# Optimization experiments

Hardware: AMD Instinct MI355X
Metric: run time of the kernel (lower is better)

Reference implementation:

```python
import jax, jax.numpy as jnp
import numpy as np

B, C, HW, SCALE = 8, 512, 64, 8
M = C // SCALE  # Q/K channel dim
EPS = 1e-6


def setup_inputs() -> dict:
    key = jax.random.key(0)
    ks = jax.random.split(key, 8)
    s = 0.02
    return {
        "x": jax.random.normal(ks[0], (B, C, HW, HW), dtype=jnp.float32),
        "wq": jax.random.normal(ks[1], (M, C), dtype=jnp.float32) * s,
        "bq": jax.random.normal(ks[2], (M,), dtype=jnp.float32) * s,
        "wk": jax.random.normal(ks[3], (M, C), dtype=jnp.float32) * s,
        "bk": jax.random.normal(ks[4], (M,), dtype=jnp.float32) * s,
        "wv": jax.random.normal(ks[5], (C, C), dtype=jnp.float32) * s,
        "bv": jax.random.normal(ks[6], (C,), dtype=jnp.float32) * s,
        "gamma": jax.random.normal(ks[7], (1,), dtype=jnp.float32),
    }


def reference(x, wq, bq, wk, bk, wv, bv, gamma):
    b, c, w, h = x.shape
    n = w * h
    xf = x.reshape(b, c, n)  # [B,C,N]
    # 1x1 convs == channel GEMMs
    Q = jnp.einsum('bcn,mc->bmn', xf, wq) + bq[None, :, None]  # [B,M,N]
    K = jnp.einsum('bcn,mc->bmn', xf, wk) + bk[None, :, None]  # [B,M,N]
    V = jnp.einsum('bcn,oc->bon', xf, wv) + bv[None, :, None]  # [B,C,N]
    # pooling gate: global max + global avg over spatial dims -> [B,C,1]
    gate = (jnp.max(xf, axis=-1) + jnp.mean(xf, axis=-1))[:, :, None]
    V = gate * V
    Qf = jax.nn.softplus(Q).transpose(0, 2, 1)  # [B,N,M]
    Kf = jax.nn.softplus(K)                      # [B,M,N]
    KV = jnp.einsum('bmn,bcn->bmc', Kf, V)       # [B,M,C]
    norm = 1.0 / jnp.einsum('bnm,bm->bn', Qf, jnp.sum(Kf, axis=-1) + EPS)  # [B,N]
    wval = jnp.einsum('bnm,bmc,bn->bcn', Qf, KV, norm)  # [B,C,N]
    wval = wval.reshape(b, c, h, w)
    return x + gamma * wval
```

## Files before the change

kernel.cpp:

```cpp
#include <hip/hip_runtime.h>
#include <math.h>

#define Bb 8
#define Cc 512
#define Nn 4096
#define Mm 64
#define OC 640
#define EPSf 1e-6f

typedef unsigned short ushort_t;
typedef unsigned int uint_t;
typedef __attribute__((ext_vector_type(8))) short short8;
typedef __attribute__((ext_vector_type(4))) float f32x4;

constexpr size_t OFF_GATE = 0;
constexpr size_t OFF_BCAT = OFF_GATE + (size_t)Bb * Cc;
constexpr size_t OFF_GPM  = OFF_BCAT + (size_t)OC;
constexpr size_t OFF_GPS  = OFF_GPM + (size_t)64 * Bb * Cc;
constexpr size_t OFF_WBF  = OFF_GPS + (size_t)64 * Bb * Cc;
constexpr size_t OFF_XT   = OFF_WBF + (size_t)OC * Cc / 2;
constexpr size_t OFF_QT   = OFF_XT + (size_t)Bb * Nn * Cc / 2;
constexpr size_t OFF_KBF  = OFF_QT + (size_t)Bb * Mm * Nn / 2;
constexpr size_t OFF_VBF  = OFF_KBF + (size_t)Bb * Mm * Nn / 2;
constexpr size_t OFF_KVBF = OFF_VBF + (size_t)Bb * Cc * Nn / 2;
constexpr size_t OFF_KSUM = OFF_KVBF + (size_t)Bb * Cc * Mm / 2;

__device__ __forceinline__ float softplus_f(float v) {
    return fmaxf(v, 0.f) + __logf(1.f + __expf(-fabsf(v)));
}
__device__ __forceinline__ ushort_t f2bf(float f) {
    uint_t u = __float_as_uint(f);
    uint_t r = (u + 0x7fffu + ((u >> 16) & 1u)) >> 16;
    return (ushort_t)r;
}
__device__ __forceinline__ float bf2f(ushort_t h) {
    return __uint_as_float(((uint_t)h) << 16);
}
__device__ __forceinline__ void gload_lds16(const void* g, void* l) {
    __builtin_amdgcn_global_load_lds(
        (const __attribute__((address_space(1))) unsigned int*)g,
        (__attribute__((address_space(3))) unsigned int*)l, 16, 0, 0);
}
#define BARRIER()   asm volatile("s_barrier" ::: "memory")
#define WAIT_VM(N)  asm volatile("s_waitcnt vmcnt(" #N ")" ::: "memory")

__global__ void wconv_k(const float* __restrict__ wq, const float* __restrict__ bq,
                        const float* __restrict__ wk, const float* __restrict__ bk,
                        const float* __restrict__ wv, const float* __restrict__ bv,
                        ushort_t* __restrict__ wbf, float* __restrict__ bcat) {
    int i = blockIdx.x * 256 + threadIdx.x;
    if (i < OC * Cc) {
        int o = i / Cc, c = i % Cc;
        float v;
        if (o < Mm)            v = wq[o * Cc + c];
        else if (o < 2 * Mm)   v = wk[(o - Mm) * Cc + c];
        else                   v = wv[(o - 2 * Mm) * Cc + c];
        wbf[i] = f2bf(v);
    }
    if (i < OC) {
        float v;
        if (i < Mm)            v = bq[i];
        else if (i < 2 * Mm)   v = bk[i - Mm];
        else                   v = bv[i - 2 * Mm];
        bcat[i] = v;
    }
}

__global__ __launch_bounds__(256) void xtrans_k(const float* __restrict__ x, ushort_t* __restrict__ xT,
                                                float* __restrict__ gpm, float* __restrict__ gps) {
    const int nb = blockIdx.x * 64;
    const int cb = blockIdx.y * 64;
    const int b  = blockIdx.z;
    __shared__ float Xt[64][65];
    __shared__ float pmx[4][64], psm[4][64];
    const int t = threadIdx.x;
    #pragma unroll
    for (int it = 0; it < 4; it++) {
        int cl = it * 16 + (t >> 4);
        int n0 = (t & 15) * 4;
        float4 v = *(const float4*)(x + ((size_t)b * Cc + cb + cl) * Nn + nb + n0);
        Xt[cl][n0 + 0] = v.x;
        Xt[cl][n0 + 1] = v.y;
        Xt[cl][n0 + 2] = v.z;
        Xt[cl][n0 + 3] = v.w;
    }
    __syncthreads();
    #pragma unroll
    for (int r = 0; r < 8; r++) {
        int nl = (t >> 5) + r * 8;
        int c0 = (t & 31) * 2;
        uint_t pk = (uint_t)f2bf(Xt[c0][nl]) | ((uint_t)f2bf(Xt[c0 + 1][nl]) << 16);
        *(uint_t*)(xT + ((size_t)b * Nn + nb + nl) * Cc + cb + c0) = pk;
    }
    {
        int cl = t & 63, q = t >> 6;
        float mx = -3.4e38f, sm = 0.f;
        #pragma unroll
        for (int j = 0; j < 16; j++) {
            float v = Xt[cl][q * 16 + j];
            mx = fmaxf(mx, v); sm += v;
        }
        pmx[q][cl] = mx; psm[q][cl] = sm;
    }
    __syncthreads();
    if (t < 64) {
        float mx = fmaxf(fmaxf(pmx[0][t], pmx[1][t]), fmaxf(pmx[2][t], pmx[3][t]));
        float sm = psm[0][t] + psm[1][t] + psm[2][t] + psm[3][t];
        size_t idx = (size_t)blockIdx.x * (Bb * Cc) + (size_t)b * Cc + cb + t;
        gpm[idx] = mx;
        gps[idx] = sm;
    }
}

__global__ void gatered_k(const float* __restrict__ gpm, const float* __restrict__ gps,
                          float* __restrict__ gate) {
    int bc = blockIdx.x;
    int l = threadIdx.x;
    float mx = gpm[(size_t)l * (Bb * Cc) + bc];
    float sm = gps[(size_t)l * (Bb * Cc) + bc];
    #pragma unroll
    for (int off = 32; off; off >>= 1) {
        mx = fmaxf(mx, __shfl_xor(mx, off));
        sm += __shfl_xor(sm, off);
    }
    if (l == 0) gate[bc] = mx + sm * (1.f / Nn);
}

__global__ __launch_bounds__(256, 4) void qkv_mfma_k(const ushort_t* __restrict__ wbf,
                                                     const ushort_t* __restrict__ xT,
                                                     const float* __restrict__ bcat,
                                                     ushort_t* __restrict__ QT,
                                                     ushort_t* __restrict__ Kbf,
                                                     ushort_t* __restrict__ Vbf) {
    const int nb  = blockIdx.x * 128;
    const int oty = blockIdx.y;
    const int b   = blockIdx.z;
    __shared__ ushort_t At[3][2048];
    __shared__ ushort_t Bt[3][4096];
    const int tid  = threadIdx.x;
    const int w    = tid >> 6;
    const int lane = tid & 63;
    const int wr   = w >> 1, wc = w & 1;
    const int hi   = lane >> 4, lo = lane & 15;
    const int rA   = tid >> 2;
    const int kc   = (((tid & 3) ^ ((tid >> 3) & 3)) * 8);
    const int sx   = (hi ^ ((lo >> 1) & 3)) * 8;
    const ushort_t* xb = xT + ((size_t)b * Nn + nb) * Cc;
    const ushort_t* wb = wbf + (size_t)oty * 64 * Cc;

    f32x4 acc[2][4] = {};

    auto stage = [&](int buf, int kb) {
        gload_lds16(wb + (size_t)rA * Cc + kb + kc,        &At[buf][w * 512]);
        gload_lds16(xb + (size_t)rA * Cc + kb + kc,        &Bt[buf][w * 512]);
        gload_lds16(xb + (size_t)(64 + rA) * Cc + kb + kc, &Bt[buf][2048 + w * 512]);
    };
    auto compute = [&](int buf) {
        short8 a[2], bfr[4];
        #pragma unroll
        for (int mi = 0; mi < 2; mi++)
            a[mi] = *(const short8*)(&At[buf][(wr * 32 + mi * 16 + lo) * 32 + sx]);
        #pragma unroll
        for (int ni = 0; ni < 4; ni++)
            bfr[ni] = *(const short8*)(&Bt[buf][(wc * 64 + ni * 16 + lo) * 32 + sx]);
        #pragma unroll
        for (int mi = 0; mi < 2; mi++)
            #pragma unroll
            for (int ni = 0; ni < 4; ni++)
                acc[mi][ni] = __builtin_amdgcn_mfma_f32_16x16x32_bf16(a[mi], bfr[ni], acc[mi][ni], 0, 0, 0);
    };

    stage(0, 0);
    stage(1, 32);
    #pragma unroll
    for (int t = 0; t < 16; ++t) {
        if (t < 15) { WAIT_VM(3); } else { WAIT_VM(0); }
        BARRIER();
        if (t + 2 < 16) stage((t + 2) % 3, (t + 2) * 32);
        compute(t % 3);
    }

    if (oty == 0) {
        ushort_t* qt = QT + ((size_t)b * Nn + nb + wc * 64) * Mm + wr * 32 + hi * 4;
        #pragma unroll
        for (int mi = 0; mi < 2; mi++) {
            const int mb = wr * 32 + mi * 16 + hi * 4;
            #pragma unroll
            for (int ni = 0; ni < 4; ni++) {
                const int n = ni * 16 + lo;
                float s0 = softplus_f(acc[mi][ni][0] + bcat[mb + 0]);
                float s1 = softplus_f(acc[mi][ni][1] + bcat[mb + 1]);
                float s2 = softplus_f(acc[mi][ni][2] + bcat[mb + 2]);
                float s3 = softplus_f(acc[mi][ni][3] + bcat[mb + 3]);
                uint2 pk;
                pk.x = (uint_t)f2bf(s0) | ((uint_t)f2bf(s1) << 16);
                pk.y = (uint_t)f2bf(s2) | ((uint_t)f2bf(s3) << 16);
                *(uint2*)(qt + (size_t)n * Mm + mi * 16) = pk;
            }
        }
    } else if (oty == 1) {
        #pragma unroll
        for (int mi = 0; mi < 2; mi++)
            #pragma unroll
            for (int r = 0; r < 4; r++) {
                const int ol = wr * 32 + mi * 16 + hi * 4 + r;
                const float bias = bcat[Mm + ol];
                ushort_t* dst = Kbf + ((size_t)b * Mm + ol) * Nn + nb + wc * 64;
                #pragma unroll
                for (int ni = 0; ni < 4; ni++)
                    dst[ni * 16 + lo] = f2bf(softplus_f(acc[mi][ni][r] + bias));
            }
    } else {
        const int cbase = (oty - 2) * 64;
        #pragma unroll
        for (int mi = 0; mi < 2; mi++)
            #pragma unroll
            for (int r = 0; r < 4; r++) {
                const int ol = wr * 32 + mi * 16 + hi * 4 + r;
                const float bias = bcat[oty * 64 + ol];
                ushort_t* dst = Vbf + ((size_t)b * Cc + cbase + ol) * Nn + nb + wc * 64;
                #pragma unroll
                for (int ni = 0; ni < 4; ni++)
                    dst[ni * 16 + lo] = f2bf(acc[mi][ni][r] + bias);
            }
    }
}

__global__ __launch_bounds__(256) void ksum_k(const ushort_t* __restrict__ Kbf, float* __restrict__ Ksum) {
    int bm = blockIdx.x;
    const ushort_t* row = Kbf + (size_t)bm * Nn;
    int t = threadIdx.x;
    float sm = 0.f;
    for (int i = t * 8; i < Nn; i += 2048) {
        short8 v = *(const short8*)(row + i);
        #pragma unroll
        for (int j = 0; j < 8; j++) sm += bf2f((ushort_t)v[j]);
    }
    #pragma unroll
    for (int off = 32; off; off >>= 1) sm += __shfl_xor(sm, off);
    __shared__ float ssm[4];
    if ((t & 63) == 0) ssm[t >> 6] = sm;
    __syncthreads();
    if (t == 0) Ksum[bm] = ssm[0] + ssm[1] + ssm[2] + ssm[3];
}

__global__ __launch_bounds__(256, 4) void kv_mfma_k(const ushort_t* __restrict__ Kbf,
                                                    const ushort_t* __restrict__ Vbf,
                                                    float* __restrict__ KVpart) {
    const int cb = blockIdx.x * 128;
    const int split = blockIdx.y;
    const int b = blockIdx.z;
    __shared__ ushort_t Vt[3][4096];
    __shared__ ushort_t Kt[3][2048];
    const int tid = threadIdx.x;
    const int w = tid >> 6, lane = tid & 63;
    const int hi = lane >> 4, lo = lane & 15;
    const int rwl = lane >> 2;
    const int kc  = (((lane & 3) ^ ((lane >> 3) & 3)) * 8);
    const int sx  = (hi ^ ((lo >> 1) & 3)) * 8;
    const ushort_t* Vb = Vbf + (size_t)b * Cc * Nn;
    const ushort_t* Kb = Kbf + (size_t)b * Mm * Nn;
    const int nbase = split * 512;

    f32x4 acc[2][4] = {};

    auto stage = [&](int buf, int n0) {
        #pragma unroll
        for (int li = 0; li < 2; li++) {
            const int rw = (w * 2 + li) * 16 + rwl;
            gload_lds16(Vb + (size_t)(cb + rw) * Nn + n0 + kc, &Vt[buf][(w * 2 + li) * 512]);
        }
        gload_lds16(Kb + (size_t)(w * 16 + rwl) * Nn + n0 + kc, &Kt[buf][w * 512]);
    };
    auto compute = [&](int buf) {
        short8 a[2], bv[4];
        #pragma unroll
        for (int mi = 0; mi < 2; mi++)
            a[mi] = *(const short8*)(&Vt[buf][(w * 32 + mi * 16 + lo) * 32 + sx]);
        #pragma unroll
        for (int ni = 0; ni < 4; ni++)
            bv[ni] = *(const short8*)(&Kt[buf][(ni * 16 + lo) * 32 + sx]);
        #pragma unroll
        for (int mi = 0; mi < 2; mi++)
            #pragma unroll
            for (int ni = 0; ni < 4; ni++)
                acc[mi][ni] = __builtin_amdgcn_mfma_f32_16x16x32_bf16(a[mi], bv[ni], acc[mi][ni], 0, 0, 0);
    };

    stage(0, nbase);
    stage(1, nbase + 32);
    #pragma unroll
    for (int t = 0; t < 16; ++t) {
        if (t < 15) { WAIT_VM(3); } else { WAIT_VM(0); }
        BARRIER();
        if (t + 2 < 16) stage((t + 2) % 3, nbase + (t + 2) * 32);
        compute(t % 3);
    }

    float* dst = KVpart + (size_t)(split * Bb + b) * Cc * Mm;
    #pragma unroll
    for (int mi = 0; mi < 2; mi++)
        #pragma unroll
        for (int r = 0; r < 4; r++) {
            const int c = cb + w * 32 + mi * 16 + hi * 4 + r;
            #pragma unroll
            for (int ni = 0; ni < 4; ni++)
                dst[(size_t)c * Mm + ni * 16 + lo] = acc[mi][ni][r];
        }
}

__global__ __launch_bounds__(256) void kvred_k(const float* __restrict__ KVpart,
                                               const float* __restrict__ gate,
                                               ushort_t* __restrict__ KVbf) {
    int i = blockIdx.x * 256 + threadIdx.x;
    const f32x4* p = (const f32x4*)KVpart;
    f32x4 s = p[i];
    #pragma unroll
    for (int sp = 1; sp < 8; sp++) s += p[(size_t)sp * 65536 + i];
    int idx4 = i * 4;
    int b = idx4 >> 15;
    int c = (idx4 >> 6) & (Cc - 1);
    float g = gate[b * Cc + c];
    uint2 pk;
    pk.x = (uint_t)f2bf(s[0] * g) | ((uint_t)f2bf(s[1] * g) << 16);
    pk.y = (uint_t)f2bf(s[2] * g) | ((uint_t)f2bf(s[3] * g) << 16);
    *(uint2*)(KVbf + (size_t)i * 4) = pk;
}

__global__ __launch_bounds__(256, 4) void final_mfma_k(const float* __restrict__ x,
                                                       const ushort_t* __restrict__ QT,
                                                       const ushort_t* __restrict__ KVbf,
                                                       const float* __restrict__ Ksum,
                                                       const float* __restrict__ gamma,
                                                       float* __restrict__ out) {
    const int nb = blockIdx.x * 128;
    const int cb = blockIdx.y * 128;
    const int b  = blockIdx.z;
    __shared__ ushort_t Qs[128 * 64];
    __shared__ ushort_t Ks[128 * 64];
    __shared__ float ksS[Mm];
    __shared__ float nrmS[128];
    const int tid  = threadIdx.x;
    const int w    = tid >> 6;
    const int lane = tid & 63;
    const int wr   = w >> 1, wc = w & 1;
    const int hi   = lane >> 4, lo = lane & 15;
    const int lr   = lane >> 3;
    const int swz  = (((lane & 7) ^ (lr & 7)) * 8);
    const ushort_t* Qb = QT + (size_t)b * Nn * Mm;
    const ushort_t* Kb = KVbf + (size_t)b * Cc * Mm;

    #pragma unroll
    for (int p = 0; p < 4; p++) {
        const int rb = p * 32 + w * 8;
        gload_lds16(Qb + (size_t)(nb + rb + lr) * Mm + swz, &Qs[rb * 64]);
        gload_lds16(Kb + (size_t)(cb + rb + lr) * Mm + swz, &Ks[rb * 64]);
    }
    if (tid < Mm) ksS[tid] = Ksum[b * Mm + tid] + EPSf;
    __syncthreads();

    if (tid < 128) {
        const int r = tid;
        float sv = 0.f;
        #pragma unroll
        for (int s = 0; s < 8; s++) {
            short8 v = *(const short8*)(&Qs[r * 64 + ((s ^ (r & 7)) * 8)]);
            #pragma unroll
            for (int e = 0; e < 8; e++) sv += bf2f((ushort_t)v[e]) * ksS[s * 8 + e];
        }
        nrmS[r] = 1.f / sv;
    }

    f32x4 acc[4][4] = {};
    #pragma unroll
    for (int kk = 0; kk < 2; kk++) {
        short8 a[4], bfr[4];
        #pragma unroll
        for (int mi = 0; mi < 4; mi++) {
            const int row = wr * 64 + mi * 16 + lo;
            a[mi] = *(const short8*)(&Qs[row * 64 + (((kk * 4 + hi) ^ (lo & 7)) * 8)]);
        }
        #pragma unroll
        for (int ni = 0; ni < 4; ni++) {
            const int row = wc * 64 + ni * 16 + lo;
            bfr[ni] = *(const short8*)(&Ks[row * 64 + (((kk * 4 + hi) ^ (lo & 7)) * 8)]);
        }
        #pragma unroll
        for (int mi = 0; mi < 4; mi++)
            #pragma unroll
            for (int ni = 0; ni < 4; ni++)
                acc[mi][ni] = __builtin_amdgcn_mfma_f32_16x16x32_bf16(a[mi], bfr[ni], acc[mi][ni], 0, 0, 0);
    }
    __syncthreads();

    const float g = gamma[0];
    #pragma unroll
    for (int mi = 0; mi < 4; mi++) {
        const int rl = wr * 64 + mi * 16 + hi * 4;
        const int n0 = nb + rl;
        float4 nrm = *(const float4*)(&nrmS[rl]);
        #pragma unroll
        for (int ni = 0; ni < 4; ni++) {
            const int c = cb + wc * 64 + ni * 16 + lo;
            size_t idx = ((size_t)b * Cc + c) * Nn + n0;
            float4 xv = *(const float4*)(x + idx);
            float4 o;
            o.x = xv.x + g * nrm.x * acc[mi][ni][0];
            o.y = xv.y + g * nrm.y * acc[mi][ni][1];
            o.z = xv.z + g * nrm.z * acc[mi][ni][2];
            o.w = xv.w + g * nrm.w * acc[mi][ni][3];
            *(float4*)(out + idx) = o;
        }
    }
}

extern "C" void kernel_launch(void* const* d_in, const int* in_sizes, int n_in,
                              void* d_out, int out_size, void* d_ws, size_t ws_size,
                              hipStream_t stream) {
    const float* x     = (const float*)d_in[0];
    const float* wq    = (const float*)d_in[1];
    const float* bq    = (const float*)d_in[2];
    const float* wk    = (const float*)d_in[3];
    const float* bk    = (const float*)d_in[4];
    const float* wv    = (const float*)d_in[5];
    const float* bv    = (const float*)d_in[6];
    const float* gamma = (const float*)d_in[7];
    float* out = (float*)d_out;
    float* ws  = (float*)d_ws;

    float*    gate   = ws + OFF_GATE;
    float*    bcat   = ws + OFF_BCAT;
    float*    gpm    = ws + OFF_GPM;
    float*    gps    = ws + OFF_GPS;
    ushort_t* wbf    = (ushort_t*)(ws + OFF_WBF);
    ushort_t* xT     = (ushort_t*)(ws + OFF_XT);
    float*    KVpart = ws + OFF_XT;
    ushort_t* QT     = (ushort_t*)(ws + OFF_QT);
    ushort_t* Kbf    = (ushort_t*)(ws + OFF_KBF);
    ushort_t* Vbf    = (ushort_t*)(ws + OFF_VBF);
    ushort_t* KVbf   = (ushort_t*)(ws + OFF_KVBF);
    float*    Ksum   = ws + OFF_KSUM;

    wconv_k<<<(OC * Cc + 255) / 256, 256, 0, stream>>>(wq, bq, wk, bk, wv, bv, wbf, bcat);
    xtrans_k<<<dim3(Nn / 64, Cc / 64, Bb), 256, 0, stream>>>(x, xT, gpm, gps);
    gatered_k<<<Bb * Cc, 64, 0, stream>>>(gpm, gps, gate);
    qkv_mfma_k<<<dim3(Nn / 128, OC / 64, Bb), 256, 0, stream>>>(wbf, xT, bcat, QT, Kbf, Vbf);
    ksum_k<<<Bb * Mm, 256, 0, stream>>>(Kbf, Ksum);
    kv_mfma_k<<<dim3(Cc / 128, 8, Bb), 256, 0, stream>>>(Kbf, Vbf, KVpart);
    kvred_k<<<(Bb * Cc * Mm / 4) / 256, 256, 0, stream>>>(KVpart, gate, KVbf);
    final_mfma_k<<<dim3(Nn / 128, Cc / 128, Bb), 256, 0, stream>>>(x, QT, KVbf, Ksum, gamma, out);
}
```

Baseline: 119.0 us.

## Enlarge QKV projection GEMM tile to 128x256 with 512-thread blocks

The QKV projection GEMM now uses 128-row by 256-column tiles computed by 8 waves, each holding a 64x64 accumulator, replacing 64x128 tiles with 4 waves. Each block reuses loaded weight and activation data across more outputs, so global and LDS traffic per FLOP drops and the grid shrinks from 2560 to 640 blocks. The epilogue is reorganised so the first output tile writes Q from one half of the waves and K from the other. In exchange the block uses twice the LDS and more accumulator registers, which can lower occupancy, and the larger grid granularity may leave some CUs idle.

```diff
diff --git a/kernel.cpp b/kernel.cpp
--- a/kernel.cpp
+++ b/kernel.cpp
@@ -126,45 +126,45 @@
     if (l == 0) gate[bc] = mx + sm * (1.f / Nn);
 }
 
-__global__ __launch_bounds__(256, 4) void qkv_mfma_k(const ushort_t* __restrict__ wbf,
+__global__ __launch_bounds__(512, 4) void qkv_mfma_k(const ushort_t* __restrict__ wbf,
                                                      const ushort_t* __restrict__ xT,
                                                      const float* __restrict__ bcat,
                                                      ushort_t* __restrict__ QT,
                                                      ushort_t* __restrict__ Kbf,
                                                      ushort_t* __restrict__ Vbf) {
-    const int nb  = blockIdx.x * 128;
-    const int oty = blockIdx.y;
-    const int b   = blockIdx.z;
-    __shared__ ushort_t At[3][2048];
-    __shared__ ushort_t Bt[3][4096];
+    const int nb = blockIdx.x * 256;
+    const int oy = blockIdx.y;
+    const int b  = blockIdx.z;
+    __shared__ ushort_t At[3][4096];
+    __shared__ ushort_t Bt[3][8192];
     const int tid  = threadIdx.x;
     const int w    = tid >> 6;
     const int lane = tid & 63;
-    const int wr   = w >> 1, wc = w & 1;
+    const int wm   = w >> 2, wn = w & 3;
     const int hi   = lane >> 4, lo = lane & 15;
     const int rA   = tid >> 2;
     const int kc   = (((tid & 3) ^ ((tid >> 3) & 3)) * 8);
     const int sx   = (hi ^ ((lo >> 1) & 3)) * 8;
     const ushort_t* xb = xT + ((size_t)b * Nn + nb) * Cc;
-    const ushort_t* wb = wbf + (size_t)oty * 64 * Cc;
-
-    f32x4 acc[2][4] = {};
+    const ushort_t* wb = wbf + (size_t)oy * 128 * Cc;
+
+    f32x4 acc[4][4] = {};
 
     auto stage = [&](int buf, int kb) {
-        gload_lds16(wb + (size_t)rA * Cc + kb + kc,        &At[buf][w * 512]);
-        gload_lds16(xb + (size_t)rA * Cc + kb + kc,        &Bt[buf][w * 512]);
-        gload_lds16(xb + (size_t)(64 + rA) * Cc + kb + kc, &Bt[buf][2048 + w * 512]);
+        gload_lds16(wb + (size_t)rA * Cc + kb + kc,         &At[buf][w * 512]);
+        gload_lds16(xb + (size_t)rA * Cc + kb + kc,         &Bt[buf][w * 512]);
+        gload_lds16(xb + (size_t)(128 + rA) * Cc + kb + kc, &Bt[buf][4096 + w * 512]);
     };
     auto compute = [&](int buf) {
-        short8 a[2], bfr[4];
-        #pragma unroll
-        for (int mi = 0; mi < 2; mi++)
-            a[mi] = *(const short8*)(&At[buf][(wr * 32 + mi * 16 + lo) * 32 + sx]);
+        short8 a[4], bfr[4];
+        #pragma unroll
+        for (int mi = 0; mi < 4; mi++)
+            a[mi] = *(const short8*)(&At[buf][(wm * 64 + mi * 16 + lo) * 32 + sx]);
         #pragma unroll
         for (int ni = 0; ni < 4; ni++)
-            bfr[ni] = *(const short8*)(&Bt[buf][(wc * 64 + ni * 16 + lo) * 32 + sx]);
-        #pragma unroll
-        for (int mi = 0; mi < 2; mi++)
+            bfr[ni] = *(const short8*)(&Bt[buf][(wn * 64 + ni * 16 + lo) * 32 + sx]);
+        #pragma unroll
+        for (int mi = 0; mi < 4; mi++)
             #pragma unroll
             for (int ni = 0; ni < 4; ni++)
                 acc[mi][ni] = __builtin_amdgcn_mfma_f32_16x16x32_bf16(a[mi], bfr[ni], acc[mi][ni], 0, 0, 0);
@@ -180,45 +180,47 @@
         compute(t % 3);
     }
 
-    if (oty == 0) {
-        ushort_t* qt = QT + ((size_t)b * Nn + nb + wc * 64) * Mm + wr * 32 + hi * 4;
-        #pragma unroll
-        for (int mi = 0; mi < 2; mi++) {
-            const int mb = wr * 32 + mi * 16 + hi * 4;
-            #pragma unroll
-            for (int ni = 0; ni < 4; ni++) {
-                const int n = ni * 16 + lo;
-                float s0 = softplus_f(acc[mi][ni][0] + bcat[mb + 0]);
-                float s1 = softplus_f(acc[mi][ni][1] + bcat[mb + 1]);
-                float s2 = softplus_f(acc[mi][ni][2] + bcat[mb + 2]);
-                float s3 = softplus_f(acc[mi][ni][3] + bcat[mb + 3]);
-                uint2 pk;
-                pk.x = (uint_t)f2bf(s0) | ((uint_t)f2bf(s1) << 16);
-                pk.y = (uint_t)f2bf(s2) | ((uint_t)f2bf(s3) << 16);
-                *(uint2*)(qt + (size_t)n * Mm + mi * 16) = pk;
+    if (oy == 0) {
+        if (wm == 0) {
+            ushort_t* qt = QT + ((size_t)b * Nn + nb + wn * 64) * Mm;
+            #pragma unroll
+            for (int mi = 0; mi < 4; mi++) {
+                const int mb = mi * 16 + hi * 4;
+                #pragma unroll
+                for (int ni = 0; ni < 4; ni++) {
+                    const int n = ni * 16 + lo;
+                    float s0 = softplus_f(acc[mi][ni][0] + bcat[mb + 0]);
+                    float s1 = softplus_f(acc[mi][ni][1] + bcat[mb + 1]);
+                    float s2 = softplus_f(acc[mi][ni][2] + bcat[mb + 2]);
+                    float s3 = softplus_f(acc[mi][ni][3] + bcat[mb + 3]);
+                    uint2 pk;
+                    pk.x = (uint_t)f2bf(s0) | ((uint_t)f2bf(s1) << 16);
+                    pk.y = (uint_t)f2bf(s2) | ((uint_t)f2bf(s3) << 16);
+                    *(uint2*)(qt + (size_t)n * Mm + mb) = pk;
+                }
             }
-        }
-    } else if (oty == 1) {
-        #pragma unroll
-        for (int mi = 0; mi < 2; mi++)
+        } else {
+            #pragma unroll
+            for (int mi = 0; mi < 4; mi++)
+                #pragma unroll
+                for (int r = 0; r < 4; r++) {
+                    const int ol = mi * 16 + hi * 4 + r;
+                    const float bias = bcat[Mm + ol];
+                    ushort_t* dst = Kbf + ((size_t)b * Mm + ol) * Nn + nb + wn * 64;
+                    #pragma unroll
+                    for (int ni = 0; ni < 4; ni++)
+                        dst[ni * 16 + lo] = f2bf(softplus_f(acc[mi][ni][r] + bias));
+                }
+        }
+    } else {
+        const int cbase = (oy - 1) * 128 + wm * 64;
+        #pragma unroll
+        for (int mi = 0; mi < 4; mi++)
             #pragma unroll
             for (int r = 0; r < 4; r++) {
-                const int ol = wr * 32 + mi * 16 + hi * 4 + r;
-                const float bias = bcat[Mm + ol];
-                ushort_t* dst = Kbf + ((size_t)b * Mm + ol) * Nn + nb + wc * 64;
-                #pragma unroll
-                for (int ni = 0; ni < 4; ni++)
-                    dst[ni * 16 + lo] = f2bf(softplus_f(acc[mi][ni][r] + bias));
-            }
-    } else {
-        const int cbase = (oty - 2) * 64;
-        #pragma unroll
-        for (int mi = 0; mi < 2; mi++)
-            #pragma unroll
-            for (int r = 0; r < 4; r++) {
-                const int ol = wr * 32 + mi * 16 + hi * 4 + r;
-                const float bias = bcat[oty * 64 + ol];
-                ushort_t* dst = Vbf + ((size_t)b * Cc + cbase + ol) * Nn + nb + wc * 64;
+                const int c = cbase + mi * 16 + hi * 4 + r;
+                const float bias = bcat[2 * Mm + c];
+                ushort_t* dst = Vbf + ((size_t)b * Cc + c) * Nn + nb + wn * 64;
                 #pragma unroll
                 for (int ni = 0; ni < 4; ni++)
                     dst[ni * 16 + lo] = f2bf(acc[mi][ni][r] + bias);
@@ -444,7 +446,7 @@
     wconv_k<<<(OC * Cc + 255) / 256, 256, 0, stream>>>(wq, bq, wk, bk, wv, bv, wbf, bcat);
     xtrans_k<<<dim3(Nn / 64, Cc / 64, Bb), 256, 0, stream>>>(x, xT, gpm, gps);
     gatered_k<<<Bb * Cc, 64, 0, stream>>>(gpm, gps, gate);
-    qkv_mfma_k<<<dim3(Nn / 128, OC / 64, Bb), 256, 0, stream>>>(wbf, xT, bcat, QT, Kbf, Vbf);
+    qkv_mfma_k<<<dim3(Nn / 256, 5, Bb), 512, 0, stream>>>(wbf, xT, bcat, QT, Kbf, Vbf);
     ksum_k<<<Bb * Mm, 256, 0, stream>>>(Kbf, Ksum);
     kv_mfma_k<<<dim3(Cc / 128, 8, Bb), 256, 0, stream>>>(Kbf, Vbf, KVpart);
     kvred_k<<<(Bb * Cc * Mm / 4) / 256, 256, 0, stream>>>(KVpart, gate, KVbf);
```

Result: faster. 115.2 us (-3.2%).
